# Performance work log

Measured on AMD Instinct MI355X. Metric: run time of the kernel, lower is better.

The kernel has to match this reference:

```python
import jax, jax.numpy as jnp
import numpy as np

B, S, SQ, N, DIN, H, A, O = 32, 1024, 32, 128, 128, 256, 100, 2000
MEM_COUNT, ANS_COUNT = 3, 2


def _gru_cell(x, h, w_ih, w_hh, b_ih, b_hh):
    # PyTorch GRUCell math
    gi = x @ w_ih.T + b_ih
    gh = h @ w_hh.T + b_hh
    i_r, i_z, i_n = jnp.split(gi, 3, axis=-1)
    h_r, h_z, h_n = jnp.split(gh, 3, axis=-1)
    r = jax.nn.sigmoid(i_r + h_r)
    z = jax.nn.sigmoid(i_z + h_z)
    n = jnp.tanh(i_n + r * h_n)
    return (1.0 - z) * n + z * h


def _gru_seq(x, h0, w_ih, w_hh, b_ih, b_hh):
    def step(h, xt):
        hn = _gru_cell(xt, h, w_ih, w_hh, b_ih, b_hh)
        return hn, hn
    hT, ys = jax.lax.scan(step, h0, jnp.swapaxes(x, 0, 1))
    return jnp.swapaxes(ys, 0, 1), hT


def setup_inputs() -> dict:
    key = jax.random.key(0)
    ks = iter(jax.random.split(key, 40))
    def U(shape, a=0.05):
        return jax.random.uniform(next(ks), shape, minval=-a, maxval=a, dtype=jnp.float32)
    inp = {}
    inp['c'] = jax.random.normal(next(ks), (B, S, DIN), dtype=jnp.float32)
    inp['q'] = jax.random.normal(next(ks), (B, SQ, DIN), dtype=jnp.float32)
    inp['i_state'] = jnp.zeros((1, B, H), jnp.float32)
    inp['q_state'] = jnp.zeros((1, B, H), jnp.float32)
    for p in ['in', 'qe']:
        inp[p + '_w_ih'] = U((3 * H, DIN)); inp[p + '_w_hh'] = U((3 * H, H))
        inp[p + '_b_ih'] = U((3 * H,)); inp[p + '_b_hh'] = U((3 * H,))
    inp['att_weight'] = U((H, H))
    inp['att_w1'] = U((A, 7 * H + 2)); inp['att_b1'] = U((A,))
    inp['att_w2'] = U((1, A)); inp['att_b2'] = U((1,))
    inp['mem_w_ih'] = U((3 * H, H)); inp['mem_w_hh'] = U((3 * H, H))
    inp['mem_b_ih'] = U((3 * H,)); inp['mem_b_hh'] = U((3 * H,))
    inp['out_w'] = U((O, H)); inp['out_b'] = U((O,))
    inp['ans_w_ih'] = U((3 * H, O + H)); inp['ans_w_hh'] = U((3 * H, H))
    inp['ans_b_ih'] = U((3 * H,)); inp['ans_b_hh'] = U((3 * H,))
    inp['c_index'] = jnp.sort(jax.random.randint(next(ks), (B, N), 0, S), axis=1)
    inp['len_c'] = jax.random.randint(next(ks), (B,), 1, N + 1)
    return inp


def reference(c, q, i_state, q_state, in_w_ih, in_w_hh, in_b_ih, in_b_hh,
              qe_w_ih, qe_w_hh, qe_b_ih, qe_b_hh, att_weight,
              att_w1, att_b1, att_w2, att_b2,
              mem_w_ih, mem_w_hh, mem_b_ih, mem_b_hh,
              out_w, out_b, ans_w_ih, ans_w_hh, ans_b_ih, ans_b_hh,
              c_index, len_c):
    # input / question GRU encoders (dropout omitted: eval mode)
    c_out, _ = _gru_seq(c, i_state[0], in_w_ih, in_w_hh, in_b_ih, in_b_hh)
    _, q_hT = _gru_seq(q, q_state[0], qe_w_ih, qe_w_hh, qe_b_ih, qe_b_hh)
    q_h = q_hT[:, None, :]                                   # [B,1,H]
    # gather sentence-end hidden states: [B,N,H]
    c_sel = jnp.take_along_axis(c_out, c_index[:, :, None], axis=1)
    n_sent = c_index.shape[1]
    mask = jnp.arange(n_sent)[None, :] < len_c[:, None]      # [B,N]
    cw = c_sel @ att_weight                                   # [B,N,H] (fixed across hops)
    m = q_h
    att_list = []
    for _ in range(MEM_COUNT):
        dot_q = (cw * q_h).sum(-1)                            # [B,N]
        dot_m = (cw * m).sum(-1)                              # [B,N]
        feats = jnp.concatenate([
            c_sel, jnp.broadcast_to(m, c_sel.shape), jnp.broadcast_to(q_h, c_sel.shape),
            c_sel * q_h, c_sel * m, jnp.abs(c_sel - q_h), jnp.abs(c_sel - m),
            dot_q[..., None], dot_m[..., None]], axis=2)      # [B,N,7H+2]
        h1 = jnp.tanh(feats @ att_w1.T + att_b1)
        scores = (h1 @ att_w2.T + att_b2)[..., 0]             # [B,N]
        p = jax.nn.softmax(jnp.where(mask, scores, -jnp.inf), axis=1)
        p = jnp.where(mask, p, 0.0)                           # zero-pad like pad_sequence
        att_list.append(p[..., None])
        e = (c_sel * p[..., None]).sum(1)                     # [B,H]
        m = _gru_cell(e, m[:, 0, :], mem_w_ih, mem_w_hh, mem_b_ih, mem_b_hh)[:, None, :]
    msq = m[:, 0, :]
    for _ in range(ANS_COUNT):
        y = jax.nn.softmax(msq @ out_w.T + out_b, axis=1)
        msq = _gru_cell(jnp.concatenate([y, q_hT], axis=1), msq,
                        ans_w_ih, ans_w_hh, ans_b_ih, ans_b_hh)
    y = jax.nn.softmax(msq @ out_w.T + out_b, axis=1)
    return y, jnp.stack(att_list)
```

## Files before the change

### kernel.cpp

```cpp
#include <hip/hip_runtime.h>
#include <cstdint>
#include <cstddef>

typedef short bf16x8 __attribute__((ext_vector_type(8)));
typedef float f32x4 __attribute__((ext_vector_type(4)));
typedef int   i32x4 __attribute__((ext_vector_type(4)));

#define DEV static __device__ __forceinline__

DEV unsigned short f2bf(float x){
  union{float f; unsigned int u;} v; v.f = x;
  unsigned int r = (v.u + 0x7FFFu + ((v.u>>16)&1u)) >> 16;
  return (unsigned short)r;
}
DEV float bf2f(unsigned short h){
  union{unsigned int u; float f;} v; v.u = ((unsigned int)h)<<16;
  return v.f;
}
DEV float bfsel(int dw, int hi){
  union{unsigned int u; float f;} v;
  v.u = hi ? ((unsigned int)dw & 0xFFFF0000u) : ((unsigned int)dw << 16);
  return v.f;
}
DEV float sigm_f(float x){ return __builtin_amdgcn_rcpf(1.0f + __expf(-x)); }
DEV float tanh_f(float x){ return 2.0f*__builtin_amdgcn_rcpf(1.0f + __expf(-2.0f*x)) - 1.0f; }

__global__ void k_f2bf(const float* __restrict__ src, unsigned short* __restrict__ dst, int n){
  int i = blockIdx.x*256 + threadIdx.x;
  if(i<n) dst[i] = f2bf(src[i]);
}

__global__ void k_transpose(const float* __restrict__ in, float* __restrict__ out, int R, int C){
  int i = blockIdx.x*256 + threadIdx.x;
  if(i < R*C){ int r = i/C, c = i - r*C; out[(size_t)c*R + r] = in[i]; }
}

__global__ void k_attw1(const float* __restrict__ w1, unsigned short* __restrict__ dst){
  int i = blockIdx.x*256 + threadIdx.x;
  if(i < 128*1824){
    int r = i/1824, cc = i - r*1824;
    float v = (r<100 && cc<1794)? w1[r*1794 + cc] : 0.0f;
    dst[i] = f2bf(v);
  }
}

__global__ void k_attwT(const float* __restrict__ aw, unsigned short* __restrict__ dst){
  int i = blockIdx.x*256 + threadIdx.x;
  if(i<65536){ int n = i>>8, k = i&255; dst[i] = f2bf(aw[k*256 + n]); }
}

__global__ void k_b1pad(const float* __restrict__ b1, float* __restrict__ dst){
  int i = threadIdx.x; if(i<128) dst[i] = (i<100)? b1[i] : 0.0f;
}

__global__ void k_copy(const float* __restrict__ s, float* __restrict__ d, int n){
  int i = blockIdx.x*256+threadIdx.x; if(i<n) d[i]=s[i];
}

__global__ __launch_bounds__(256) void k_gemm_bf16(
    const unsigned short* __restrict__ A, const unsigned short* __restrict__ Bt,
    int K, const float* __restrict__ bias, int act,
    float* __restrict__ outf, unsigned short* __restrict__ outbf, int ldc)
{
  int lane = threadIdx.x & 63, wave = threadIdx.x >> 6;
  int m_base = blockIdx.x*64 + (wave>>1)*32;
  int n_base = blockIdx.y*64 + (wave&1)*32;
  int cl = lane & 15, q4 = lane >> 4;
  f32x4 acc00={0.f,0.f,0.f,0.f}, acc01=acc00, acc10=acc00, acc11=acc00;
  const int kf_n = K >> 5;
  for(int kf=0; kf<kf_n; kf++){
    int ko = kf*32 + q4*8;
    bf16x8 a0 = *(const bf16x8*)(A + (size_t)(m_base+cl)*K + ko);
    bf16x8 a1 = *(const bf16x8*)(A + (size_t)(m_base+16+cl)*K + ko);
    bf16x8 b0 = *(const bf16x8*)(Bt + (size_t)(n_base+cl)*K + ko);
    bf16x8 b1 = *(const bf16x8*)(Bt + (size_t)(n_base+16+cl)*K + ko);
    acc00 = __builtin_amdgcn_mfma_f32_16x16x32_bf16(a0,b0,acc00,0,0,0);
    acc01 = __builtin_amdgcn_mfma_f32_16x16x32_bf16(a0,b1,acc01,0,0,0);
    acc10 = __builtin_amdgcn_mfma_f32_16x16x32_bf16(a1,b0,acc10,0,0,0);
    acc11 = __builtin_amdgcn_mfma_f32_16x16x32_bf16(a1,b1,acc11,0,0,0);
  }
  #pragma unroll
  for(int mt=0; mt<2; mt++){
    #pragma unroll
    for(int nt=0; nt<2; nt++){
      f32x4 av = (mt==0)? (nt==0?acc00:acc01) : (nt==0?acc10:acc11);
      int col = n_base + nt*16 + cl;
      float bv = bias? bias[col] : 0.0f;
      #pragma unroll
      for(int r=0;r<4;r++){
        int row = m_base + mt*16 + q4*4 + r;
        float v = av[r] + bv;
        if(act) v = tanh_f(v);
        if(outbf) outbf[(size_t)row*ldc + col] = f2bf(v);
        else      outf [(size_t)row*ldc + col] = v;
      }
    }
  }
}

__global__ __launch_bounds__(256) void k_gemm_gi(
    const unsigned short* __restrict__ A, const unsigned short* __restrict__ Bt,
    const float* __restrict__ bias, unsigned short* __restrict__ gi_out, int ss)
{
  int lane = threadIdx.x & 63, wave = threadIdx.x >> 6;
  int m_base = blockIdx.x*64 + (wave>>1)*32;
  int n_base = blockIdx.y*64 + (wave&1)*32;
  int cl = lane & 15, q4 = lane >> 4;
  f32x4 acc00={0.f,0.f,0.f,0.f}, acc01=acc00, acc10=acc00, acc11=acc00;
  for(int kf=0; kf<4; kf++){
    int ko = kf*32 + q4*8;
    bf16x8 a0 = *(const bf16x8*)(A + (size_t)(m_base+cl)*128 + ko);
    bf16x8 a1 = *(const bf16x8*)(A + (size_t)(m_base+16+cl)*128 + ko);
    bf16x8 b0 = *(const bf16x8*)(Bt + (size_t)(n_base+cl)*128 + ko);
    bf16x8 b1 = *(const bf16x8*)(Bt + (size_t)(n_base+16+cl)*128 + ko);
    acc00 = __builtin_amdgcn_mfma_f32_16x16x32_bf16(a0,b0,acc00,0,0,0);
    acc01 = __builtin_amdgcn_mfma_f32_16x16x32_bf16(a0,b1,acc01,0,0,0);
    acc10 = __builtin_amdgcn_mfma_f32_16x16x32_bf16(a1,b0,acc10,0,0,0);
    acc11 = __builtin_amdgcn_mfma_f32_16x16x32_bf16(a1,b1,acc11,0,0,0);
  }
  const int tmask = (1<<ss) - 1;
  #pragma unroll
  for(int mt=0; mt<2; mt++){
    #pragma unroll
    for(int nt=0; nt<2; nt++){
      f32x4 av = (mt==0)? (nt==0?acc00:acc01) : (nt==0?acc10:acc11);
      int col = n_base + nt*16 + cl;
      float bv = bias[col];
      int g = col >> 8, rem = col & 255;
      int w = rem >> 5, s = (rem>>4)&1, cl2 = rem & 15;
      #pragma unroll
      for(int r=0;r<4;r++){
        int arow = m_base + mt*16 + q4*4 + r;
        int t = arow & tmask, b = arow >> ss;
        int blk = b >> 4, brow = b & 15;
        int lane2 = (brow>>2)*16 + cl2, rc = brow & 3;
        size_t idx = ((((size_t)t*2 + blk)*8 + w)*64 + lane2)*24 + g*8 + s*4 + rc;
        gi_out[idx] = f2bf(av[r] + bv);
      }
    }
  }
}

__global__ __launch_bounds__(512,1) void k_gru_rec(
    const unsigned short* __restrict__ whh_c, const unsigned short* __restrict__ whh_q,
    const unsigned short* __restrict__ gi_c,  const unsigned short* __restrict__ gi_q,
    const float* __restrict__ bhh_c, const float* __restrict__ bhh_q,
    const float* __restrict__ h0_c,  const float* __restrict__ h0_q,
    float* __restrict__ c_out, float* __restrict__ q_hT)
{
  __shared__ unsigned short hb0[16*264];
  __shared__ unsigned short hb1[16*264];

  const int blk = blockIdx.x;
  const bool isq = blk >= 2;
  const int cls = isq? blk-2 : blk;
  const int b0 = cls * 16;
  const unsigned short* W  = isq? whh_q : whh_c;
  const unsigned short* GI = isq? gi_q  : gi_c;
  const float* bhh = isq? bhh_q : bhh_c;
  const float* h0  = isq? h0_q  : h0_c;
  const int steps  = isq? 32 : 1024;

  const int tid = threadIdx.x;
  const int lane = tid & 63, wave = tid >> 6;
  const int cl = lane & 15, q4 = lane >> 4;

  bf16x8 Bf[3][2][8];
  #pragma unroll
  for(int g=0; g<3; g++)
    #pragma unroll
    for(int s=0; s<2; s++){
      const unsigned short* wrow = W + (size_t)(g*256 + wave*32 + s*16 + cl)*256;
      #pragma unroll
      for(int kf=0; kf<8; kf++)
        Bf[g][s][kf] = *(const bf16x8*)(wrow + kf*32 + q4*8);
    }

  float bR[2], bZ[2], bN[2];
  #pragma unroll
  for(int s=0; s<2; s++){
    const int col = wave*32 + s*16 + cl;
    bR[s] = bhh[col]; bZ[s] = bhh[256+col]; bN[s] = bhh[512+col];
  }

  float hreg[2][4];
  #pragma unroll
  for(int s=0; s<2; s++){
    const int col = wave*32 + s*16 + cl;
    #pragma unroll
    for(int r=0; r<4; r++){
      const int row = q4*4 + r;
      float v = h0[(size_t)(b0+row)*256 + col];
      hreg[s][r] = v;
      hb0[row*264 + col] = f2bf(v);
    }
  }
  __syncthreads();

  unsigned short* hb_rd = hb0;
  unsigned short* hb_wr = hb1;

  const unsigned short* gi_lane = GI + (((size_t)cls*8 + wave)*64 + lane)*24;
  const size_t gi_tstride = (size_t)2*8*64*24;

  for(int t=0; t<steps; t++){
    const unsigned short* gp = gi_lane + (size_t)t*gi_tstride;
    i32x4 G0 = *(const i32x4*)(gp);
    i32x4 G1 = *(const i32x4*)(gp + 8);
    i32x4 G2 = *(const i32x4*)(gp + 16);

    if(!isq && t>0){
      #pragma unroll
      for(int s=0; s<2; s++){
        const int col = wave*32 + s*16 + cl;
        #pragma unroll
        for(int r=0; r<4; r++)
          c_out[((size_t)(b0+q4*4+r)*1024 + (t-1))*256 + col] = hreg[s][r];
      }
    }

    f32x4 acc[3][2];
    #pragma unroll
    for(int g=0; g<3; g++)
      #pragma unroll
      for(int s=0; s<2; s++){ f32x4 z={0.f,0.f,0.f,0.f}; acc[g][s]=z; }
    #pragma unroll
    for(int kf=0; kf<8; kf++){
      bf16x8 a = *(const bf16x8*)&hb_rd[cl*264 + kf*32 + q4*8];
      #pragma unroll
      for(int g=0; g<3; g++)
        #pragma unroll
        for(int s=0; s<2; s++)
          acc[g][s] = __builtin_amdgcn_mfma_f32_16x16x32_bf16(a, Bf[g][s][kf], acc[g][s], 0,0,0);
    }

    #pragma unroll
    for(int s=0; s<2; s++){
      const int col = wave*32 + s*16 + cl;
      #pragma unroll
      for(int r=0; r<4; r++){
        const int row = q4*4 + r;
        const int k = s*4 + r;
        float gir = bfsel(G0[k>>1], k&1);
        float giz = bfsel(G1[k>>1], k&1);
        float gin = bfsel(G2[k>>1], k&1);
        float rr = sigm_f(gir + acc[0][s][r] + bR[s]);
        float zz = sigm_f(giz + acc[1][s][r] + bZ[s]);
        float nn = tanh_f(gin + rr*(acc[2][s][r] + bN[s]));
        float x  = nn + zz*(hreg[s][r] - nn);
        hreg[s][r] = x;
        hb_wr[row*264 + col] = f2bf(x);
      }
    }
    __syncthreads();
    unsigned short* tmp = hb_rd; hb_rd = hb_wr; hb_wr = tmp;
  }

  #pragma unroll
  for(int s=0; s<2; s++){
    const int col = wave*32 + s*16 + cl;
    #pragma unroll
    for(int r=0; r<4; r++){
      const int row = q4*4 + r;
      if(!isq) c_out[((size_t)(b0+row)*1024 + (steps-1))*256 + col] = hreg[s][r];
      else     q_hT[(size_t)(b0+row)*256 + col] = hreg[s][r];
    }
  }
}

__global__ void k_gather(const float* __restrict__ c_out, const int* __restrict__ c_index,
                         float* __restrict__ c_sel, unsigned short* __restrict__ c_sel_bf){
  int row = blockIdx.x;
  int b = row >> 7, s = row & 127;
  int idx = c_index[b*128 + s];
  float v = c_out[((size_t)b*1024 + idx)*256 + threadIdx.x];
  c_sel   [(size_t)row*256 + threadIdx.x] = v;
  c_sel_bf[(size_t)row*256 + threadIdx.x] = f2bf(v);
}

__global__ void k_feats(const float* __restrict__ c_sel, const float* __restrict__ cw,
                        const float* __restrict__ m_, const float* __restrict__ qh,
                        unsigned short* __restrict__ feats){
  int row = blockIdx.x, tid = threadIdx.x;
  int b = row >> 7;
  float cs  = c_sel[(size_t)row*256 + tid];
  float mj  = m_[b*256 + tid];
  float qj  = qh[b*256 + tid];
  float cwj = cw[(size_t)row*256 + tid];
  float dq = cwj*qj, dm = cwj*mj;
  #pragma unroll
  for(int o=32;o>0;o>>=1){ dq += __shfl_down(dq,o); dm += __shfl_down(dm,o); }
  __shared__ float rq[4], rm[4];
  int lane = tid&63, wave=tid>>6;
  if(lane==0){ rq[wave]=dq; rm[wave]=dm; }
  __syncthreads();
  unsigned short* fr = feats + (size_t)row*1824;
  fr[tid]      = f2bf(cs);
  fr[256+tid]  = f2bf(mj);
  fr[512+tid]  = f2bf(qj);
  fr[768+tid]  = f2bf(cs*qj);
  fr[1024+tid] = f2bf(cs*mj);
  fr[1280+tid] = f2bf(fabsf(cs-qj));
  fr[1536+tid] = f2bf(fabsf(cs-mj));
  if(tid==0){
    float DQ = rq[0]+rq[1]+rq[2]+rq[3];
    float DM = rm[0]+rm[1]+rm[2]+rm[3];
    fr[1792]=f2bf(DQ); fr[1793]=f2bf(DM);
  }
  if(tid<30) fr[1794+tid]=0;
}

__global__ void k_scores(const float* __restrict__ h1, const float* __restrict__ w2,
                         const float* __restrict__ b2, float* __restrict__ scores){
  int row = blockIdx.x*4 + (threadIdx.x>>6);
  int lane = threadIdx.x & 63;
  float v = 0.0f;
  if(lane < 100)    v += h1[(size_t)row*128 + lane]*w2[lane];
  if(lane+64 < 100) v += h1[(size_t)row*128 + lane+64]*w2[lane+64];
  #pragma unroll
  for(int o=32;o>0;o>>=1) v += __shfl_down(v,o);
  if(lane==0) scores[row] = v + b2[0];
}

__global__ void k_softmax_e(const float* __restrict__ scores, const int* __restrict__ len_c,
                            const float* __restrict__ c_sel, float* __restrict__ out_att,
                            float* __restrict__ e){
  __shared__ float red[256];
  __shared__ float p[128];
  int b = blockIdx.x, tid = threadIdx.x;
  int L = len_c[b];
  float s = -1e30f;
  if(tid<128 && tid<L) s = scores[b*128+tid];
  red[tid]=s; __syncthreads();
  for(int o=128;o>0;o>>=1){ if(tid<o) red[tid]=fmaxf(red[tid],red[tid+o]); __syncthreads(); }
  float mx = red[0]; __syncthreads();
  float ex = (tid<128 && tid<L)? __expf(s-mx) : 0.0f;
  red[tid]=ex; __syncthreads();
  for(int o=128;o>0;o>>=1){ if(tid<o) red[tid]+=red[tid+o]; __syncthreads(); }
  float inv = 1.0f/red[0];
  if(tid<128){ float pv = ex*inv; p[tid]=pv; out_att[b*128+tid]=pv; }
  __syncthreads();
  float acc = 0.0f;
  for(int si=0; si<128; si++) acc += p[si]*c_sel[((size_t)b*128+si)*256 + tid];
  e[b*256+tid] = acc;
}

__global__ void k_gru_cell(const float* __restrict__ x1, int len1,
                           const float* __restrict__ x2, int len2,
                           const float* __restrict__ hprev,
                           const float* __restrict__ wihT, const float* __restrict__ whhT,
                           const float* __restrict__ bih, const float* __restrict__ bhh,
                           float* __restrict__ hout){
  __shared__ float xs[2304];
  __shared__ float hs[256];
  int m = blockIdx.x, tid = threadIdx.x;
  int Kx = len1 + len2;
  for(int i=tid;i<len1;i+=256) xs[i] = x1[(size_t)m*len1 + i];
  for(int i=tid;i<len2;i+=256) xs[len1+i] = x2[(size_t)m*len2 + i];
  hs[tid] = hprev[m*256 + tid];
  __syncthreads();
  float ar=0, az=0, an=0;
  for(int k=0;k<Kx;k++){
    float xv = xs[k];
    const float* wr = wihT + (size_t)k*768;
    ar += xv*wr[tid]; az += xv*wr[256+tid]; an += xv*wr[512+tid];
  }
  float gr=0, gz=0, gn=0;
  for(int k=0;k<256;k++){
    float hv = hs[k];
    const float* wr = whhT + (size_t)k*768;
    gr += hv*wr[tid]; gz += hv*wr[256+tid]; gn += hv*wr[512+tid];
  }
  float rr = sigm_f(ar + bih[tid]     + gr + bhh[tid]);
  float zz = sigm_f(az + bih[256+tid] + gz + bhh[256+tid]);
  float nn = tanh_f(an + bih[512+tid] + rr*(gn + bhh[512+tid]));
  hout[m*256+tid] = (1.0f-zz)*nn + zz*hs[tid];
}

__global__ void k_logits(const float* __restrict__ msq, const float* __restrict__ out_wT,
                         const float* __restrict__ out_b, float* __restrict__ ylin){
  int i = blockIdx.x*256 + threadIdx.x;
  if(i >= 32*2000) return;
  int mrow = i/2000, n = i - mrow*2000;
  float acc = out_b[n];
  const float* mr = msq + mrow*256;
  for(int k=0;k<256;k++) acc += mr[k]*out_wT[(size_t)k*2000 + n];
  ylin[i] = acc;
}

__global__ void k_softmax_o(const float* __restrict__ x, float* __restrict__ y){
  __shared__ float red[256];
  int b = blockIdx.x, tid = threadIdx.x;
  const float* xr = x + (size_t)b*2000;
  float mx = -1e30f;
  for(int i=tid;i<2000;i+=256) mx = fmaxf(mx, xr[i]);
  red[tid]=mx; __syncthreads();
  for(int o=128;o>0;o>>=1){ if(tid<o) red[tid]=fmaxf(red[tid],red[tid+o]); __syncthreads(); }
  mx = red[0]; __syncthreads();
  float sum=0.0f;
  for(int i=tid;i<2000;i+=256) sum += __expf(xr[i]-mx);
  red[tid]=sum; __syncthreads();
  for(int o=128;o>0;o>>=1){ if(tid<o) red[tid]+=red[tid+o]; __syncthreads(); }
  float inv = 1.0f/red[0];
  for(int i=tid;i<2000;i+=256) y[(size_t)b*2000+i] = __expf(xr[i]-mx)*inv;
}

extern "C" void kernel_launch(void* const* d_in, const int* in_sizes, int n_in,
                              void* d_out, int out_size, void* d_ws, size_t ws_size,
                              hipStream_t stream)
{
  const float* c        = (const float*)d_in[0];
  const float* q        = (const float*)d_in[1];
  const float* i_state  = (const float*)d_in[2];
  const float* q_state  = (const float*)d_in[3];
  const float* in_w_ih  = (const float*)d_in[4];
  const float* in_w_hh  = (const float*)d_in[5];
  const float* in_b_ih  = (const float*)d_in[6];
  const float* in_b_hh  = (const float*)d_in[7];
  const float* qe_w_ih  = (const float*)d_in[8];
  const float* qe_w_hh  = (const float*)d_in[9];
  const float* qe_b_ih  = (const float*)d_in[10];
  const float* qe_b_hh  = (const float*)d_in[11];
  const float* att_weight = (const float*)d_in[12];
  const float* att_w1   = (const float*)d_in[13];
  const float* att_b1   = (const float*)d_in[14];
  const float* att_w2   = (const float*)d_in[15];
  const float* att_b2   = (const float*)d_in[16];
  const float* mem_w_ih = (const float*)d_in[17];
  const float* mem_w_hh = (const float*)d_in[18];
  const float* mem_b_ih = (const float*)d_in[19];
  const float* mem_b_hh = (const float*)d_in[20];
  const float* out_w    = (const float*)d_in[21];
  const float* out_b    = (const float*)d_in[22];
  const float* ans_w_ih = (const float*)d_in[23];
  const float* ans_w_hh = (const float*)d_in[24];
  const float* ans_b_ih = (const float*)d_in[25];
  const float* ans_b_hh = (const float*)d_in[26];
  const int*   c_index  = (const int*)d_in[27];
  const int*   len_c    = (const int*)d_in[28];
  float* outp = (float*)d_out;

  char* wp = (char*)d_ws;
  auto take = [&](size_t nbytes)->char*{
    char* p = wp; wp += (nbytes + 255) & ~(size_t)255; return p;
  };
  unsigned short* c_bf      = (unsigned short*)take((size_t)32*1024*128*2);
  unsigned short* q_bf      = (unsigned short*)take((size_t)32*32*128*2);
  unsigned short* wih_in_bf = (unsigned short*)take(768*128*2);
  unsigned short* wih_qe_bf = (unsigned short*)take(768*128*2);
  unsigned short* whh_in_bf = (unsigned short*)take(768*256*2);
  unsigned short* whh_qe_bf = (unsigned short*)take(768*256*2);
  unsigned short* attwT_bf  = (unsigned short*)take(256*256*2);
  unsigned short* attw1_bf  = (unsigned short*)take(128*1824*2);
  float* b1pad              = (float*)take(128*4);
  float* out_wT             = (float*)take((size_t)256*2000*4);
  float* mem_wihT           = (float*)take(256*768*4);
  float* mem_whhT           = (float*)take(256*768*4);
  float* ans_wihT           = (float*)take((size_t)2256*768*4);
  float* ans_whhT           = (float*)take(256*768*4);
  unsigned short* gi_c_bf   = (unsigned short*)take((size_t)32768*768*2);
  unsigned short* gi_q_bf   = (unsigned short*)take((size_t)1024*768*2);
  float* c_out              = (float*)take((size_t)32*1024*256*4);
  float* q_hT               = (float*)take(32*256*4);
  float* c_sel              = (float*)take((size_t)4096*256*4);
  unsigned short* c_sel_bf  = (unsigned short*)take((size_t)4096*256*2);
  float* cw                 = (float*)take((size_t)4096*256*4);
  unsigned short* feats_bf  = (unsigned short*)take((size_t)4096*1824*2);
  float* h1                 = (float*)take((size_t)4096*128*4);
  float* scores             = (float*)take(4096*4);
  float* e_buf              = (float*)take(32*256*4);
  float* m_buf              = (float*)take(32*256*4);
  float* msq                = (float*)take(32*256*4);
  float* ylin               = (float*)take((size_t)32*2000*4);
  float* ybuf               = (float*)take((size_t)32*2000*4);

  k_f2bf<<<16384,256,0,stream>>>(c, c_bf, 32*1024*128);
  k_f2bf<<<512,256,0,stream>>>(q, q_bf, 32*32*128);
  k_f2bf<<<384,256,0,stream>>>(in_w_ih, wih_in_bf, 768*128);
  k_f2bf<<<384,256,0,stream>>>(qe_w_ih, wih_qe_bf, 768*128);
  k_f2bf<<<768,256,0,stream>>>(in_w_hh, whh_in_bf, 768*256);
  k_f2bf<<<768,256,0,stream>>>(qe_w_hh, whh_qe_bf, 768*256);
  k_attwT<<<256,256,0,stream>>>(att_weight, attwT_bf);
  k_attw1<<<912,256,0,stream>>>(att_w1, attw1_bf);
  k_b1pad<<<1,128,0,stream>>>(att_b1, b1pad);
  k_transpose<<<2000,256,0,stream>>>(out_w, out_wT, 2000, 256);
  k_transpose<<<768,256,0,stream>>>(mem_w_ih, mem_wihT, 768, 256);
  k_transpose<<<768,256,0,stream>>>(mem_w_hh, mem_whhT, 768, 256);
  k_transpose<<<6768,256,0,stream>>>(ans_w_ih, ans_wihT, 768, 2256);
  k_transpose<<<768,256,0,stream>>>(ans_w_hh, ans_whhT, 768, 256);

  k_gemm_gi<<<dim3(512,12),256,0,stream>>>(c_bf, wih_in_bf, in_b_ih, gi_c_bf, 10);
  k_gemm_gi<<<dim3(16,12),256,0,stream>>>(q_bf, wih_qe_bf, qe_b_ih, gi_q_bf, 5);

  k_gru_rec<<<4,512,0,stream>>>(whh_in_bf, whh_qe_bf, gi_c_bf, gi_q_bf,
                                in_b_hh, qe_b_hh, i_state, q_state, c_out, q_hT);

  k_gather<<<4096,256,0,stream>>>(c_out, c_index, c_sel, c_sel_bf);
  k_gemm_bf16<<<dim3(64,4),256,0,stream>>>(c_sel_bf, attwT_bf, 256, nullptr, 0, cw, nullptr, 256);
  k_copy<<<32,256,0,stream>>>(q_hT, m_buf, 32*256);

  for(int it=0; it<3; it++){
    k_feats<<<4096,256,0,stream>>>(c_sel, cw, m_buf, q_hT, feats_bf);
    k_gemm_bf16<<<dim3(64,2),256,0,stream>>>(feats_bf, attw1_bf, 1824, b1pad, 1, h1, nullptr, 128);
    k_scores<<<1024,256,0,stream>>>(h1, att_w2, att_b2, scores);
    k_softmax_e<<<32,256,0,stream>>>(scores, len_c, c_sel, outp + 64000 + it*4096, e_buf);
    k_gru_cell<<<32,256,0,stream>>>(e_buf, 256, nullptr, 0, m_buf,
                                    mem_wihT, mem_whhT, mem_b_ih, mem_b_hh, m_buf);
  }

  k_copy<<<32,256,0,stream>>>(m_buf, msq, 32*256);
  for(int it=0; it<2; it++){
    k_logits<<<250,256,0,stream>>>(msq, out_wT, out_b, ylin);
    k_softmax_o<<<32,256,0,stream>>>(ylin, ybuf);
    k_gru_cell<<<32,256,0,stream>>>(ybuf, 2000, q_hT, 256, msq,
                                    ans_wihT, ans_whhT, ans_b_ih, ans_b_hh, msq);
  }
  k_logits<<<250,256,0,stream>>>(msq, out_wT, out_b, ylin);
  k_softmax_o<<<32,256,0,stream>>>(ylin, outp);
}
```

Baseline: 3.061 ms.

## Overlap GRU gate math for first column half with second half MFMAs

Splits the recurrent GRU MFMA loop into two column halves, so the sigmoid/tanh gate math for the first half is interleaved with the MFMAs of the second half. Biases are folded into the accumulator initialisation. Rounding uses the hardware packed bf16 convert instruction, and the __syncthreads is replaced with an explicit waitcnt plus s_barrier. The aim is to hide transcendental latency on the sequential critical path of the GRU scan. In exchange it reloads the A fragments from LDS twice and ties the kernel to gfx950-specific inline asm.

```diff
diff --git a/kernel.cpp b/kernel.cpp
--- a/kernel.cpp
+++ b/kernel.cpp
@@ -219,40 +219,82 @@
       }
     }
 
-    f32x4 acc[3][2];
-    #pragma unroll
-    for(int g=0; g<3; g++)
-      #pragma unroll
-      for(int s=0; s<2; s++){ f32x4 z={0.f,0.f,0.f,0.f}; acc[g][s]=z; }
+    f32x4 aR0 = {bR[0],bR[0],bR[0],bR[0]};
+    f32x4 aZ0 = {bZ[0],bZ[0],bZ[0],bZ[0]};
+    f32x4 aN0 = {bN[0],bN[0],bN[0],bN[0]};
+    f32x4 aR1 = {bR[1],bR[1],bR[1],bR[1]};
+    f32x4 aZ1 = {bZ[1],bZ[1],bZ[1],bZ[1]};
+    f32x4 aN1 = {bN[1],bN[1],bN[1],bN[1]};
+
     #pragma unroll
     for(int kf=0; kf<8; kf++){
       bf16x8 a = *(const bf16x8*)&hb_rd[cl*264 + kf*32 + q4*8];
-      #pragma unroll
-      for(int g=0; g<3; g++)
-        #pragma unroll
-        for(int s=0; s<2; s++)
-          acc[g][s] = __builtin_amdgcn_mfma_f32_16x16x32_bf16(a, Bf[g][s][kf], acc[g][s], 0,0,0);
-    }
-
-    #pragma unroll
-    for(int s=0; s<2; s++){
-      const int col = wave*32 + s*16 + cl;
+      aR0 = __builtin_amdgcn_mfma_f32_16x16x32_bf16(a, Bf[0][0][kf], aR0, 0,0,0);
+      aZ0 = __builtin_amdgcn_mfma_f32_16x16x32_bf16(a, Bf[1][0][kf], aZ0, 0,0,0);
+      aN0 = __builtin_amdgcn_mfma_f32_16x16x32_bf16(a, Bf[2][0][kf], aN0, 0,0,0);
+    }
+
+    float x0[4];
+    #pragma unroll
+    for(int kf=0; kf<8; kf++){
+      bf16x8 a = *(const bf16x8*)&hb_rd[cl*264 + kf*32 + q4*8];
+      aR1 = __builtin_amdgcn_mfma_f32_16x16x32_bf16(a, Bf[0][1][kf], aR1, 0,0,0);
+      aZ1 = __builtin_amdgcn_mfma_f32_16x16x32_bf16(a, Bf[1][1][kf], aZ1, 0,0,0);
+      aN1 = __builtin_amdgcn_mfma_f32_16x16x32_bf16(a, Bf[2][1][kf], aN1, 0,0,0);
+      if(kf & 1){
+        const int r = kf >> 1;
+        float gir = bfsel(G0[r>>1], r&1);
+        float giz = bfsel(G1[r>>1], r&1);
+        float gin = bfsel(G2[r>>1], r&1);
+        float rr = sigm_f(gir + aR0[r]);
+        float zz = sigm_f(giz + aZ0[r]);
+        float nn = tanh_f(gin + rr*aN0[r]);
+        float x  = nn + zz*(hreg[0][r] - nn);
+        hreg[0][r] = x;
+        x0[r] = x;
+      }
+    }
+
+    {
+      const int col = wave*32 + cl;
+      unsigned int d01, d23;
+      asm("v_cvt_pk_bf16_f32 %0, %1, %2" : "=v"(d01) : "v"(x0[0]), "v"(x0[1]));
+      asm("v_cvt_pk_bf16_f32 %0, %1, %2" : "=v"(d23) : "v"(x0[2]), "v"(x0[3]));
+      hb_wr[(q4*4+0)*264 + col] = (unsigned short)(d01 & 0xFFFFu);
+      hb_wr[(q4*4+1)*264 + col] = (unsigned short)(d01 >> 16);
+      hb_wr[(q4*4+2)*264 + col] = (unsigned short)(d23 & 0xFFFFu);
+      hb_wr[(q4*4+3)*264 + col] = (unsigned short)(d23 >> 16);
+    }
+
+    {
+      float x1[4];
       #pragma unroll
       for(int r=0; r<4; r++){
-        const int row = q4*4 + r;
-        const int k = s*4 + r;
+        const int k = 4 + r;
         float gir = bfsel(G0[k>>1], k&1);
         float giz = bfsel(G1[k>>1], k&1);
         float gin = bfsel(G2[k>>1], k&1);
-        float rr = sigm_f(gir + acc[0][s][r] + bR[s]);
-        float zz = sigm_f(giz + acc[1][s][r] + bZ[s]);
-        float nn = tanh_f(gin + rr*(acc[2][s][r] + bN[s]));
-        float x  = nn + zz*(hreg[s][r] - nn);
-        hreg[s][r] = x;
-        hb_wr[row*264 + col] = f2bf(x);
+        float rr = sigm_f(gir + aR1[r]);
+        float zz = sigm_f(giz + aZ1[r]);
+        float nn = tanh_f(gin + rr*aN1[r]);
+        float x  = nn + zz*(hreg[1][r] - nn);
+        hreg[1][r] = x;
+        x1[r] = x;
       }
-    }
-    __syncthreads();
+      const int col = wave*32 + 16 + cl;
+      unsigned int d01, d23;
+      asm("v_cvt_pk_bf16_f32 %0, %1, %2" : "=v"(d01) : "v"(x1[0]), "v"(x1[1]));
+      asm("v_cvt_pk_bf16_f32 %0, %1, %2" : "=v"(d23) : "v"(x1[2]), "v"(x1[3]));
+      hb_wr[(q4*4+0)*264 + col] = (unsigned short)(d01 & 0xFFFFu);
+      hb_wr[(q4*4+1)*264 + col] = (unsigned short)(d01 >> 16);
+      hb_wr[(q4*4+2)*264 + col] = (unsigned short)(d23 & 0xFFFFu);
+      hb_wr[(q4*4+3)*264 + col] = (unsigned short)(d23 >> 16);
+    }
+
+    asm volatile("s_waitcnt lgkmcnt(0)" ::: "memory");
+    __builtin_amdgcn_s_barrier();
+    asm volatile("" ::: "memory");
+
     unsigned short* tmp = hb_rd; hb_rd = hb_wr; hb_wr = tmp;
   }
 
```

Result: slower. 4.568 ms (+49.2%).

## Split GRU recurrence across 16 waves, one column tile per wave

Applied to the files above, without the earlier changes.

The sequential GRU recurrence kernel now launches 1024 threads (16 waves) per block instead of 512. Each wave owns a single 16-column tile per gate rather than two, which halves the per-wave MFMA chain and elementwise work on every time step. The hidden-side bias is also folded into the MFMA accumulator's initial value instead of being added afterwards. The cost is a barrier across twice as many waves each step and tighter register budgets under the 1024-thread launch bound.

```diff
diff --git a/kernel.cpp b/kernel.cpp
--- a/kernel.cpp
+++ b/kernel.cpp
@@ -5,6 +5,7 @@
 typedef short bf16x8 __attribute__((ext_vector_type(8)));
 typedef float f32x4 __attribute__((ext_vector_type(4)));
 typedef int   i32x4 __attribute__((ext_vector_type(4)));
+typedef int   i32x2 __attribute__((ext_vector_type(2)));
 
 #define DEV static __device__ __forceinline__
 
@@ -141,7 +142,7 @@
   }
 }
 
-__global__ __launch_bounds__(512,1) void k_gru_rec(
+__global__ __launch_bounds__(1024,1) void k_gru_rec(
     const unsigned short* __restrict__ whh_c, const unsigned short* __restrict__ whh_q,
     const unsigned short* __restrict__ gi_c,  const unsigned short* __restrict__ gi_q,
     const float* __restrict__ bhh_c, const float* __restrict__ bhh_q,
@@ -163,108 +164,82 @@
 
   const int tid = threadIdx.x;
   const int lane = tid & 63, wave = tid >> 6;
+  const int w8 = wave & 7, sg = wave >> 3;
   const int cl = lane & 15, q4 = lane >> 4;
-
-  bf16x8 Bf[3][2][8];
-  #pragma unroll
-  for(int g=0; g<3; g++)
+  const int col = w8*32 + sg*16 + cl;
+
+  bf16x8 Bf[3][8];
+  #pragma unroll
+  for(int g=0; g<3; g++){
+    const unsigned short* wrow = W + (size_t)(g*256 + col)*256;
     #pragma unroll
-    for(int s=0; s<2; s++){
-      const unsigned short* wrow = W + (size_t)(g*256 + wave*32 + s*16 + cl)*256;
+    for(int kf=0; kf<8; kf++)
+      Bf[g][kf] = *(const bf16x8*)(wrow + kf*32 + q4*8);
+  }
+
+  const float bR = bhh[col], bZ = bhh[256+col], bN = bhh[512+col];
+
+  float hreg[4];
+  #pragma unroll
+  for(int r=0; r<4; r++){
+    const int row = q4*4 + r;
+    float v = h0[(size_t)(b0+row)*256 + col];
+    hreg[r] = v;
+    hb0[row*264 + col] = f2bf(v);
+  }
+  __syncthreads();
+
+  unsigned short* hb_rd = hb0;
+  unsigned short* hb_wr = hb1;
+
+  const unsigned short* gi_lane = GI + (((size_t)cls*8 + w8)*64 + lane)*24 + sg*4;
+  const size_t gi_tstride = (size_t)2*8*64*24;
+
+  for(int t=0; t<steps; t++){
+    const unsigned short* gp = gi_lane + (size_t)t*gi_tstride;
+    i32x2 G0 = *(const i32x2*)(gp);
+    i32x2 G1 = *(const i32x2*)(gp + 8);
+    i32x2 G2 = *(const i32x2*)(gp + 16);
+
+    if(!isq && t>0){
       #pragma unroll
-      for(int kf=0; kf<8; kf++)
-        Bf[g][s][kf] = *(const bf16x8*)(wrow + kf*32 + q4*8);
+      for(int r=0; r<4; r++)
+        c_out[((size_t)(b0+q4*4+r)*1024 + (t-1))*256 + col] = hreg[r];
     }
 
-  float bR[2], bZ[2], bN[2];
-  #pragma unroll
-  for(int s=0; s<2; s++){
-    const int col = wave*32 + s*16 + cl;
-    bR[s] = bhh[col]; bZ[s] = bhh[256+col]; bN[s] = bhh[512+col];
-  }
-
-  float hreg[2][4];
-  #pragma unroll
-  for(int s=0; s<2; s++){
-    const int col = wave*32 + s*16 + cl;
+    f32x4 aR = {bR,bR,bR,bR};
+    f32x4 aZ = {bZ,bZ,bZ,bZ};
+    f32x4 aN = {bN,bN,bN,bN};
+    #pragma unroll
+    for(int kf=0; kf<8; kf++){
+      bf16x8 a = *(const bf16x8*)&hb_rd[cl*264 + kf*32 + q4*8];
+      aR = __builtin_amdgcn_mfma_f32_16x16x32_bf16(a, Bf[0][kf], aR, 0,0,0);
+      aZ = __builtin_amdgcn_mfma_f32_16x16x32_bf16(a, Bf[1][kf], aZ, 0,0,0);
+      aN = __builtin_amdgcn_mfma_f32_16x16x32_bf16(a, Bf[2][kf], aN, 0,0,0);
+    }
+
     #pragma unroll
     for(int r=0; r<4; r++){
       const int row = q4*4 + r;
-      float v = h0[(size_t)(b0+row)*256 + col];
-      hreg[s][r] = v;
-      hb0[row*264 + col] = f2bf(v);
-    }
-  }
-  __syncthreads();
-
-  unsigned short* hb_rd = hb0;
-  unsigned short* hb_wr = hb1;
-
-  const unsigned short* gi_lane = GI + (((size_t)cls*8 + wave)*64 + lane)*24;
-  const size_t gi_tstride = (size_t)2*8*64*24;
-
-  for(int t=0; t<steps; t++){
-    const unsigned short* gp = gi_lane + (size_t)t*gi_tstride;
-    i32x4 G0 = *(const i32x4*)(gp);
-    i32x4 G1 = *(const i32x4*)(gp + 8);
-    i32x4 G2 = *(const i32x4*)(gp + 16);
-
-    if(!isq && t>0){
-      #pragma unroll
-      for(int s=0; s<2; s++){
-        const int col = wave*32 + s*16 + cl;
-        #pragma unroll
-        for(int r=0; r<4; r++)
-          c_out[((size_t)(b0+q4*4+r)*1024 + (t-1))*256 + col] = hreg[s][r];
-      }
-    }
-
-    f32x4 acc[3][2];
-    #pragma unroll
-    for(int g=0; g<3; g++)
-      #pragma unroll
-      for(int s=0; s<2; s++){ f32x4 z={0.f,0.f,0.f,0.f}; acc[g][s]=z; }
-    #pragma unroll
-    for(int kf=0; kf<8; kf++){
-      bf16x8 a = *(const bf16x8*)&hb_rd[cl*264 + kf*32 + q4*8];
-      #pragma unroll
-      for(int g=0; g<3; g++)
-        #pragma unroll
-        for(int s=0; s<2; s++)
-          acc[g][s] = __builtin_amdgcn_mfma_f32_16x16x32_bf16(a, Bf[g][s][kf], acc[g][s], 0,0,0);
-    }
-
-    #pragma unroll
-    for(int s=0; s<2; s++){
-      const int col = wave*32 + s*16 + cl;
-      #pragma unroll
-      for(int r=0; r<4; r++){
-        const int row = q4*4 + r;
-        const int k = s*4 + r;
-        float gir = bfsel(G0[k>>1], k&1);
-        float giz = bfsel(G1[k>>1], k&1);
-        float gin = bfsel(G2[k>>1], k&1);
-        float rr = sigm_f(gir + acc[0][s][r] + bR[s]);
-        float zz = sigm_f(giz + acc[1][s][r] + bZ[s]);
-        float nn = tanh_f(gin + rr*(acc[2][s][r] + bN[s]));
-        float x  = nn + zz*(hreg[s][r] - nn);
-        hreg[s][r] = x;
-        hb_wr[row*264 + col] = f2bf(x);
-      }
+      float gir = bfsel(G0[r>>1], r&1);
+      float giz = bfsel(G1[r>>1], r&1);
+      float gin = bfsel(G2[r>>1], r&1);
+      float rr = sigm_f(gir + aR[r]);
+      float zz = sigm_f(giz + aZ[r]);
+      float nn = tanh_f(gin + rr*aN[r]);
+      float x  = nn + zz*(hreg[r] - nn);
+      hreg[r] = x;
+      hb_wr[row*264 + col] = f2bf(x);
     }
     __syncthreads();
     unsigned short* tmp = hb_rd; hb_rd = hb_wr; hb_wr = tmp;
   }
 
   #pragma unroll
-  for(int s=0; s<2; s++){
-    const int col = wave*32 + s*16 + cl;
-    #pragma unroll
-    for(int r=0; r<4; r++){
-      const int row = q4*4 + r;
-      if(!isq) c_out[((size_t)(b0+row)*1024 + (steps-1))*256 + col] = hreg[s][r];
-      else     q_hT[(size_t)(b0+row)*256 + col] = hreg[s][r];
-    }
+  for(int r=0; r<4; r++){
+    const int row = q4*4 + r;
+    if(!isq) c_out[((size_t)(b0+row)*1024 + (steps-1))*256 + col] = hreg[r];
+    else     q_hT[(size_t)(b0+row)*256 + col] = hreg[r];
   }
 }
 
@@ -492,8 +467,8 @@
   k_gemm_gi<<<dim3(512,12),256,0,stream>>>(c_bf, wih_in_bf, in_b_ih, gi_c_bf, 10);
   k_gemm_gi<<<dim3(16,12),256,0,stream>>>(q_bf, wih_qe_bf, qe_b_ih, gi_q_bf, 5);
 
-  k_gru_rec<<<4,512,0,stream>>>(whh_in_bf, whh_qe_bf, gi_c_bf, gi_q_bf,
-                                in_b_hh, qe_b_hh, i_state, q_state, c_out, q_hT);
+  k_gru_rec<<<4,1024,0,stream>>>(whh_in_bf, whh_qe_bf, gi_c_bf, gi_q_bf,
+                                 in_b_hh, qe_b_hh, i_state, q_state, c_out, q_hT);
 
   k_gather<<<4096,256,0,stream>>>(c_out, c_index, c_sel, c_sel_bf);
   k_gemm_bf16<<<dim3(64,4),256,0,stream>>>(c_sel_bf, attwT_bf, 256, nullptr, 0, cw, nullptr, 256);
```

Result: slower. 4.716 ms (+54.0%).

## Transpose recurrent GRU MFMA outputs for vectorized stores and bias-initialized accumulators

Applied to the files above, without the earlier changes.

The recurrent GRU kernel swaps the MFMA operand order so each lane holds four consecutive hidden columns for one batch row instead of four rows of one column. This allows 16-byte vector stores of the hidden state to c_out, packed bf16 conversion with a single 8-byte LDS write per subtile, and vector loads of bias and h0. The hh bias is folded into the accumulator initialization, which removes per-step adds. The input-projection kernel's output layout is permuted to match the new lane mapping, so the two kernels have to stay consistent.

```diff
diff --git a/kernel.cpp b/kernel.cpp
--- a/kernel.cpp
+++ b/kernel.cpp
@@ -5,6 +5,7 @@
 typedef short bf16x8 __attribute__((ext_vector_type(8)));
 typedef float f32x4 __attribute__((ext_vector_type(4)));
 typedef int   i32x4 __attribute__((ext_vector_type(4)));
+typedef unsigned int u32x2 __attribute__((ext_vector_type(2)));
 
 #define DEV static __device__ __forceinline__
 
@@ -127,14 +128,14 @@
       int col = n_base + nt*16 + cl;
       float bv = bias[col];
       int g = col >> 8, rem = col & 255;
-      int w = rem >> 5, s = (rem>>4)&1, cl2 = rem & 15;
+      int w = rem >> 5, s = (rem>>4)&1, q4o = (rem>>2)&3, ro = rem&3;
       #pragma unroll
       for(int r=0;r<4;r++){
         int arow = m_base + mt*16 + q4*4 + r;
         int t = arow & tmask, b = arow >> ss;
         int blk = b >> 4, brow = b & 15;
-        int lane2 = (brow>>2)*16 + cl2, rc = brow & 3;
-        size_t idx = ((((size_t)t*2 + blk)*8 + w)*64 + lane2)*24 + g*8 + s*4 + rc;
+        int lane2 = q4o*16 + brow;
+        size_t idx = ((((size_t)t*2 + blk)*8 + w)*64 + lane2)*24 + g*8 + s*4 + ro;
         gi_out[idx] = f2bf(av[r] + bv);
       }
     }
@@ -176,23 +177,22 @@
         Bf[g][s][kf] = *(const bf16x8*)(wrow + kf*32 + q4*8);
     }
 
-  float bR[2], bZ[2], bN[2];
+  f32x4 bv[3][2];
+  #pragma unroll
+  for(int g=0; g<3; g++)
+    #pragma unroll
+    for(int s=0; s<2; s++)
+      bv[g][s] = *(const f32x4*)&bhh[g*256 + wave*32 + s*16 + q4*4];
+
+  float hreg[2][4];
   #pragma unroll
   for(int s=0; s<2; s++){
-    const int col = wave*32 + s*16 + cl;
-    bR[s] = bhh[col]; bZ[s] = bhh[256+col]; bN[s] = bhh[512+col];
-  }
-
-  float hreg[2][4];
-  #pragma unroll
-  for(int s=0; s<2; s++){
-    const int col = wave*32 + s*16 + cl;
+    const int colb = wave*32 + s*16 + q4*4;
+    f32x4 v = *(const f32x4*)&h0[(size_t)(b0+cl)*256 + colb];
     #pragma unroll
     for(int r=0; r<4; r++){
-      const int row = q4*4 + r;
-      float v = h0[(size_t)(b0+row)*256 + col];
-      hreg[s][r] = v;
-      hb0[row*264 + col] = f2bf(v);
+      hreg[s][r] = v[r];
+      hb0[cl*264 + colb + r] = f2bf(v[r]);
     }
   }
   __syncthreads();
@@ -212,10 +212,8 @@
     if(!isq && t>0){
       #pragma unroll
       for(int s=0; s<2; s++){
-        const int col = wave*32 + s*16 + cl;
-        #pragma unroll
-        for(int r=0; r<4; r++)
-          c_out[((size_t)(b0+q4*4+r)*1024 + (t-1))*256 + col] = hreg[s][r];
+        f32x4 hv = {hreg[s][0], hreg[s][1], hreg[s][2], hreg[s][3]};
+        *(f32x4*)&c_out[((size_t)(b0+cl)*1024 + (t-1))*256 + wave*32 + s*16 + q4*4] = hv;
       }
     }
 
@@ -223,7 +221,7 @@
     #pragma unroll
     for(int g=0; g<3; g++)
       #pragma unroll
-      for(int s=0; s<2; s++){ f32x4 z={0.f,0.f,0.f,0.f}; acc[g][s]=z; }
+      for(int s=0; s<2; s++) acc[g][s] = bv[g][s];
     #pragma unroll
     for(int kf=0; kf<8; kf++){
       bf16x8 a = *(const bf16x8*)&hb_rd[cl*264 + kf*32 + q4*8];
@@ -231,26 +229,30 @@
       for(int g=0; g<3; g++)
         #pragma unroll
         for(int s=0; s<2; s++)
-          acc[g][s] = __builtin_amdgcn_mfma_f32_16x16x32_bf16(a, Bf[g][s][kf], acc[g][s], 0,0,0);
+          acc[g][s] = __builtin_amdgcn_mfma_f32_16x16x32_bf16(Bf[g][s][kf], a, acc[g][s], 0,0,0);
     }
 
     #pragma unroll
     for(int s=0; s<2; s++){
-      const int col = wave*32 + s*16 + cl;
+      const int colb = wave*32 + s*16 + q4*4;
+      float x[4];
       #pragma unroll
       for(int r=0; r<4; r++){
-        const int row = q4*4 + r;
         const int k = s*4 + r;
         float gir = bfsel(G0[k>>1], k&1);
         float giz = bfsel(G1[k>>1], k&1);
         float gin = bfsel(G2[k>>1], k&1);
-        float rr = sigm_f(gir + acc[0][s][r] + bR[s]);
-        float zz = sigm_f(giz + acc[1][s][r] + bZ[s]);
-        float nn = tanh_f(gin + rr*(acc[2][s][r] + bN[s]));
-        float x  = nn + zz*(hreg[s][r] - nn);
-        hreg[s][r] = x;
-        hb_wr[row*264 + col] = f2bf(x);
+        float rr = sigm_f(gir + acc[0][s][r]);
+        float zz = sigm_f(giz + acc[1][s][r]);
+        float nn = tanh_f(gin + rr*acc[2][s][r]);
+        x[r] = nn + zz*(hreg[s][r] - nn);
+        hreg[s][r] = x[r];
       }
+      unsigned int d01, d23;
+      asm("v_cvt_pk_bf16_f32 %0, %1, %2" : "=v"(d01) : "v"(x[0]), "v"(x[1]));
+      asm("v_cvt_pk_bf16_f32 %0, %1, %2" : "=v"(d23) : "v"(x[2]), "v"(x[3]));
+      u32x2 dv = {d01, d23};
+      *(u32x2*)&hb_wr[cl*264 + colb] = dv;
     }
     __syncthreads();
     unsigned short* tmp = hb_rd; hb_rd = hb_wr; hb_wr = tmp;
@@ -258,13 +260,10 @@
 
   #pragma unroll
   for(int s=0; s<2; s++){
-    const int col = wave*32 + s*16 + cl;
-    #pragma unroll
-    for(int r=0; r<4; r++){
-      const int row = q4*4 + r;
-      if(!isq) c_out[((size_t)(b0+row)*1024 + (steps-1))*256 + col] = hreg[s][r];
-      else     q_hT[(size_t)(b0+row)*256 + col] = hreg[s][r];
-    }
+    const int colb = wave*32 + s*16 + q4*4;
+    f32x4 hv = {hreg[s][0], hreg[s][1], hreg[s][2], hreg[s][3]};
+    if(!isq) *(f32x4*)&c_out[((size_t)(b0+cl)*1024 + (steps-1))*256 + colb] = hv;
+    else     *(f32x4*)&q_hT[(size_t)(b0+cl)*256 + colb] = hv;
   }
 }
 
```

After: 4.686 ms. 1.53x slower.
